# Optimization experiments

Hardware: AMD Instinct MI355X
Metric: run time of the kernel (lower is better)

Reference implementation:

```python
import jax, jax.numpy as jnp
import numpy as np

B, L, D, H, NC = 32, 1024, 256, 512, 16


def setup_inputs() -> dict:
    key = jax.random.key(0)
    ks = jax.random.split(key, 8)
    s_in = 1.0 / np.sqrt(D)
    s_h = 1.0 / np.sqrt(H)
    return {
        "x": jax.random.normal(ks[0], (B, L, D), jnp.float32),
        "W0": jax.random.normal(ks[1], (D, 4 * H), jnp.float32) * s_in,
        "b0": jnp.zeros((2 * H,), jnp.float32),
        "W1": jax.random.normal(ks[2], (H, 3 * H), jnp.float32) * s_h,
        "b1": jnp.zeros((2 * H,), jnp.float32),
        "W2": jax.random.normal(ks[3], (H, 3 * H), jnp.float32) * s_h,
        "b2": jnp.zeros((2 * H,), jnp.float32),
        "W3": jax.random.normal(ks[4], (H, 3 * H), jnp.float32) * s_h,
        "b3": jnp.zeros((2 * H,), jnp.float32),
        "Wp": jax.random.normal(ks[5], (H, H), jnp.float32) * s_h,
        "bp": jnp.zeros((H,), jnp.float32),
        "Wc": jax.random.normal(ks[6], (H, NC), jnp.float32) * s_h,
        "bc": jnp.zeros((NC,), jnp.float32),
    }


def _sru_layer(h, W, b, first):
    # h: (B, L, Din); W: (Din, kH); b: (2H,)
    k = 4 if first else 3
    Hh = W.shape[1] // k
    U = jnp.einsum('bld,dk->blk', h, W)  # (B, L, kH)
    if first:
        xt, fpre, rpre, xres = jnp.split(U, 4, axis=-1)
    else:
        xt, fpre, rpre = jnp.split(U, 3, axis=-1)
        xres = h
    bf, br = jnp.split(b, 2)
    f = jax.nn.sigmoid(fpre + bf)  # forget gate (B, L, H)
    r = jax.nn.sigmoid(rpre + br)  # reset/highway gate

    def step(c, inp):
        f_t, x_t = inp
        c = f_t * c + (1.0 - f_t) * x_t
        return c, c

    c0 = jnp.zeros((h.shape[0], Hh), h.dtype)
    _, c_seq = jax.lax.scan(step, c0, (jnp.swapaxes(f, 0, 1), jnp.swapaxes(xt, 0, 1)))
    c_seq = jnp.swapaxes(c_seq, 0, 1)  # (B, L, H)
    out = r * c_seq + (1.0 - r) * xres  # highway output
    return out, c_seq[:, -1, :]


def reference(x, W0, b0, W1, b1, W2, b2, W3, b3, Wp, bp, Wc, bc):
    h = x
    finals = []
    for W, b, first in ((W0, b0, True), (W1, b1, False), (W2, b2, False), (W3, b3, False)):
        h, cT = _sru_layer(h, W, b, first)
        finals.append(cT)
    hidden = jnp.stack(finals)  # (num_layers, B, H)
    projected = h[:, -1, :] @ Wp + bp
    output = projected @ Wc + bc
    return output, h, hidden
```

## Files before the change

kernel.cpp:

```cpp
#include <hip/hip_runtime.h>

#define DEV_INLINE __device__ __forceinline__

typedef __attribute__((ext_vector_type(8))) short bf16x8;
typedef __attribute__((ext_vector_type(4))) float f32x4;

DEV_INLINE unsigned short f2bf(float f) {
  union { float f; unsigned u; } v; v.f = f;
  unsigned r = v.u + 0x7FFFu + ((v.u >> 16) & 1u);
  return (unsigned short)(r >> 16);
}
DEV_INLINE float bf2f(unsigned short u) {
  union { unsigned u; float f; } v; v.u = ((unsigned)u) << 16;
  return v.f;
}
DEV_INLINE float sigmoidf_(float x) { return 1.0f / (1.0f + __expf(-x)); }

DEV_INLINE void gload_lds16(const void* g, void* l) {
  __builtin_amdgcn_global_load_lds(
      (const __attribute__((address_space(1))) void*)(g),
      (__attribute__((address_space(3))) void*)(l), 16, 0, 0);
}

__global__ __launch_bounds__(256)
void f32_to_bf16_kernel(const float* __restrict__ in, unsigned short* __restrict__ out, int n4) {
  int i = blockIdx.x * blockDim.x + threadIdx.x;
  if (i >= n4) return;
  const float4 v = reinterpret_cast<const float4*>(in)[i];
  ushort4 o;
  o.x = f2bf(v.x); o.y = f2bf(v.y); o.z = f2bf(v.z); o.w = f2bf(v.w);
  reinterpret_cast<ushort4*>(out)[i] = o;
}

__global__ __launch_bounds__(256)
void transpose_bf16_kernel(const float* __restrict__ W, unsigned short* __restrict__ Wt,
                           int K, int N) {
  __shared__ float tile[32][33];
  const int tx = threadIdx.x, ty = threadIdx.y;
  const int kb = blockIdx.x * 32, nb = blockIdx.y * 32;
  #pragma unroll
  for (int i = 0; i < 32; i += 8)
    tile[ty + i][tx] = W[(size_t)(kb + ty + i) * N + (nb + tx)];
  __syncthreads();
  #pragma unroll
  for (int i = 0; i < 32; i += 8)
    Wt[(size_t)(nb + ty + i) * K + (kb + tx)] = f2bf(tile[tx][ty + i]);
}

__global__ __launch_bounds__(256, 2)
void gemm_gate_kernel(const unsigned short* __restrict__ A,
                      const unsigned short* __restrict__ Bt,
                      const float* __restrict__ bias,
                      unsigned short* __restrict__ U,
                      int N, int K, int NTN) {
  __shared__ short smem[2 * 128 * 64];
  short* As = smem;
  short* Bs = smem + 128 * 64;

  const int tid = threadIdx.x;
  const int lane = tid & 63;
  const int l15 = lane & 15;
  const int l4 = lane >> 4;
  const int w = tid >> 6;
  const int wr = (w >> 1) * 64;
  const int wc = (w & 1) * 64;

  const int nwg = gridDim.x;
  const int cpx = nwg >> 3;
  const int swz = (blockIdx.x & 7) * cpx + (blockIdx.x >> 3);
  const int mtile = swz / NTN;
  const int ntile = swz - mtile * NTN;
  const int m0 = mtile * 128;
  const int n0 = ntile * 128;

  f32x4 acc[4][4];
  #pragma unroll
  for (int i = 0; i < 4; ++i)
    #pragma unroll
    for (int j = 0; j < 4; ++j)
      acc[i][j] = (f32x4){0.f, 0.f, 0.f, 0.f};

  const unsigned short* Abase = A + (size_t)m0 * K;
  const unsigned short* Bbase = Bt + (size_t)n0 * K;
  const int nsteps = K >> 6;

  for (int t = 0; t < nsteps; ++t) {
    const int k0 = t * 64;
    #pragma unroll
    for (int it = 0; it < 4; ++it) {
      int c = it * 256 + tid;
      int row = c >> 3, sl = c & 7;
      int ks = sl ^ (row & 7);
      gload_lds16(Abase + (size_t)row * K + (k0 + ks * 8), &As[c * 8]);
    }
    #pragma unroll
    for (int it = 0; it < 4; ++it) {
      int c = it * 256 + tid;
      int row = c >> 3, sl = c & 7;
      int ks = sl ^ (row & 7);
      gload_lds16(Bbase + (size_t)row * K + (k0 + ks * 8), &Bs[c * 8]);
    }
    __syncthreads();

    const bf16x8* As8 = (const bf16x8*)As;
    const bf16x8* Bs8 = (const bf16x8*)Bs;
    #pragma unroll
    for (int kk = 0; kk < 2; ++kk) {
      bf16x8 af[4], bfr[4];
      #pragma unroll
      for (int i = 0; i < 4; ++i) {
        int r = wr + i * 16 + l15;
        int phys = (kk * 4 + l4) ^ (r & 7);
        af[i] = As8[r * 8 + phys];
      }
      #pragma unroll
      for (int j = 0; j < 4; ++j) {
        int r = wc + j * 16 + l15;
        int phys = (kk * 4 + l4) ^ (r & 7);
        bfr[j] = Bs8[r * 8 + phys];
      }
      #pragma unroll
      for (int i = 0; i < 4; ++i)
        #pragma unroll
        for (int j = 0; j < 4; ++j)
          acc[i][j] = __builtin_amdgcn_mfma_f32_16x16x32_bf16(af[i], bfr[j], acc[i][j], 0, 0, 0);
    }
    __syncthreads();
  }

  short* eps = smem;
  const int EL = 144;
  #pragma unroll
  for (int p = 0; p < 2; ++p) {
    __syncthreads();
    #pragma unroll
    for (int ii = 0; ii < 2; ++ii) {
      const int i = 2 * p + ii;
      #pragma unroll
      for (int j = 0; j < 4; ++j) {
        const int cg = n0 + wc + j * 16 + l15;
        const int region = cg >> 9;
        #pragma unroll
        for (int reg = 0; reg < 4; ++reg) {
          float v = acc[i][j][reg];
          if (region == 1)      v = sigmoidf_(v + bias[cg & 511]);
          else if (region == 2) v = sigmoidf_(v + bias[512 + (cg & 511)]);
          const int lr = (wr >> 1) + ii * 16 + l4 * 4 + reg;
          const int col = (wc + j * 16 + l15) ^ (((lr >> 2) & 3) << 3);
          eps[lr * EL + col] = (short)f2bf(v);
        }
      }
    }
    __syncthreads();
    const int lr2 = tid >> 2;
    const int grow = m0 + ((lr2 >> 5) << 6) + (2 * p + ((lr2 >> 4) & 1)) * 16 + (lr2 & 15);
    const int xorv = ((lr2 >> 2) & 3) << 3;
    unsigned short* urow = U + (size_t)grow * N + n0;
    #pragma unroll
    for (int k = 0; k < 4; ++k) {
      const int col = (tid & 3) * 8 + k * 32;
      bf16x8 vv = *(const bf16x8*)&eps[lr2 * EL + (col ^ xorv)];
      *(bf16x8*)(urow + col) = vv;
    }
  }
}

__global__ __launch_bounds__(512)
void scan_kernel(const unsigned short* __restrict__ U, int N, int first,
                 const unsigned short* __restrict__ hin,
                 unsigned short* __restrict__ hout_bf,
                 float* __restrict__ hout_f32,
                 float* __restrict__ hidden) {
  const int b = blockIdx.x >> 3;
  const int hslice = blockIdx.x & 7;
  const int hv = threadIdx.x & 7;
  const int ch = threadIdx.x >> 3;
  const int h0 = (hslice << 6) + (hv << 3);
  __shared__ float sP[64 * 68];
  __shared__ float sQ[64 * 68];

  const size_t rowBase = (size_t)b * 1024 + (size_t)ch * 16;
  const unsigned short* Uxt = U + rowBase * N + h0;

  float c[8], P[8];
  #pragma unroll
  for (int j = 0; j < 8; ++j) { c[j] = 0.f; P[j] = 1.f; }
  {
    const unsigned short* px = Uxt;
    const unsigned short* pf = Uxt + 512;
    #pragma unroll 2
    for (int l = 0; l < 16; ++l) {
      bf16x8 xv = *(const bf16x8*)px;
      bf16x8 fv = *(const bf16x8*)pf;
      #pragma unroll
      for (int j = 0; j < 8; ++j) {
        float f  = bf2f((unsigned short)fv[j]);
        float xt = bf2f((unsigned short)xv[j]);
        c[j] = f * c[j] + (1.f - f) * xt;
        P[j] *= f;
      }
      px += N; pf += N;
    }
  }
  float* myP = &sP[ch * 68 + hv * 8];
  float* myQ = &sQ[ch * 68 + hv * 8];
  #pragma unroll
  for (int j = 0; j < 8; ++j) { myP[j] = P[j]; myQ[j] = c[j]; }
  __syncthreads();

  for (int s = 1; s < 64; s <<= 1) {
    float pp[8], pq[8];
    const bool act = (ch >= s);
    if (act) {
      const float* qP = &sP[(ch - s) * 68 + hv * 8];
      const float* qQ = &sQ[(ch - s) * 68 + hv * 8];
      #pragma unroll
      for (int j = 0; j < 8; ++j) { pp[j] = qP[j]; pq[j] = qQ[j]; }
    }
    __syncthreads();
    if (act) {
      #pragma unroll
      for (int j = 0; j < 8; ++j) {
        c[j] = P[j] * pq[j] + c[j];
        P[j] = P[j] * pp[j];
        myP[j] = P[j]; myQ[j] = c[j];
      }
    }
    __syncthreads();
  }

  float cc[8];
  if (ch == 0) {
    #pragma unroll
    for (int j = 0; j < 8; ++j) cc[j] = 0.f;
  } else {
    const float* qQ = &sQ[(ch - 1) * 68 + hv * 8];
    #pragma unroll
    for (int j = 0; j < 8; ++j) cc[j] = qQ[j];
  }

  const unsigned short* px = Uxt;
  const unsigned short* pf = Uxt + 512;
  const unsigned short* pr = Uxt + 1024;
  const unsigned short* pxr = first ? (Uxt + 1536) : (hin + rowBase * 512 + h0);
  const int xr_stride = first ? N : 512;
  unsigned short* ob = hout_bf ? hout_bf + rowBase * 512 + h0 : (unsigned short*)nullptr;
  float* of = hout_f32 ? hout_f32 + rowBase * 512 + h0 : (float*)nullptr;
  #pragma unroll 2
  for (int l = 0; l < 16; ++l) {
    bf16x8 xv = *(const bf16x8*)px;
    bf16x8 fv = *(const bf16x8*)pf;
    bf16x8 rv = *(const bf16x8*)pr;
    bf16x8 xrv = *(const bf16x8*)pxr;
    bf16x8 obuf;
    float o0, o1, o2, o3, o4, o5, o6, o7;
    float ofl[8];
    #pragma unroll
    for (int j = 0; j < 8; ++j) {
      float f  = bf2f((unsigned short)fv[j]);
      float xt = bf2f((unsigned short)xv[j]);
      cc[j] = f * cc[j] + (1.f - f) * xt;
      float r  = bf2f((unsigned short)rv[j]);
      float xr = bf2f((unsigned short)xrv[j]);
      float o = r * cc[j] + (1.f - r) * xr;
      obuf[j] = (short)f2bf(o);
      ofl[j] = o;
    }
    if (ob) { *(bf16x8*)ob = obuf; ob += 512; }
    if (of) {
      float4 v0 = make_float4(ofl[0], ofl[1], ofl[2], ofl[3]);
      float4 v1 = make_float4(ofl[4], ofl[5], ofl[6], ofl[7]);
      *(float4*)of = v0;
      *(float4*)(of + 4) = v1;
      of += 512;
    }
    px += N; pf += N; pr += N; pxr += xr_stride;
  }
  if (ch == 63) {
    #pragma unroll
    for (int j = 0; j < 8; ++j) hidden[(size_t)b * 512 + h0 + j] = cc[j];
  }
}

__global__ __launch_bounds__(256)
void proj_kernel(const float* __restrict__ hfull, const float* __restrict__ Wp,
                 const float* __restrict__ bp, const float* __restrict__ Wc,
                 const float* __restrict__ bc, float* __restrict__ out) {
  __shared__ float hl[512];
  __shared__ float pr[512];
  const int b = blockIdx.x, t = threadIdx.x;
  const float* hrow = hfull + ((size_t)b * 1024 + 1023) * 512;
  hl[t] = hrow[t];
  hl[t + 256] = hrow[t + 256];
  __syncthreads();
  for (int j = t; j < 512; j += 256) {
    float s = 0.f;
    for (int k = 0; k < 512; ++k) s += hl[k] * Wp[(size_t)k * 512 + j];
    pr[j] = s + bp[j];
  }
  __syncthreads();
  if (t < 16) {
    float s = 0.f;
    for (int k = 0; k < 512; ++k) s += pr[k] * Wc[k * 16 + t];
    out[b * 16 + t] = s + bc[t];
  }
}

extern "C" void kernel_launch(void* const* d_in, const int* in_sizes, int n_in,
                              void* d_out, int out_size, void* d_ws, size_t ws_size,
                              hipStream_t stream) {
  const float* x  = (const float*)d_in[0];
  const float* W0 = (const float*)d_in[1];
  const float* b0 = (const float*)d_in[2];
  const float* W1 = (const float*)d_in[3];
  const float* b1 = (const float*)d_in[4];
  const float* W2 = (const float*)d_in[5];
  const float* b2 = (const float*)d_in[6];
  const float* W3 = (const float*)d_in[7];
  const float* b3 = (const float*)d_in[8];
  const float* Wp = (const float*)d_in[9];
  const float* bp = (const float*)d_in[10];
  const float* Wc = (const float*)d_in[11];
  const float* bc = (const float*)d_in[12];

  float* out = (float*)d_out;
  float* outO = out;
  float* outH = out + 512;
  float* outHid = out + 512 + (size_t)32 * 1024 * 512;

  char* ws = (char*)d_ws;
  size_t off = 0;
  auto alloc = [&](size_t bytes) {
    void* p = ws + off;
    off += (bytes + 255) & ~(size_t)255;
    return p;
  };
  unsigned short* Wt0 = (unsigned short*)alloc((size_t)2048 * 256 * 2);
  unsigned short* Wt1 = (unsigned short*)alloc((size_t)1536 * 512 * 2);
  unsigned short* Wt2 = (unsigned short*)alloc((size_t)1536 * 512 * 2);
  unsigned short* Wt3 = (unsigned short*)alloc((size_t)1536 * 512 * 2);
  unsigned short* xbf = (unsigned short*)alloc((size_t)32768 * 256 * 2);
  unsigned short* h0  = (unsigned short*)alloc((size_t)32768 * 512 * 2);
  unsigned short* h1  = (unsigned short*)alloc((size_t)32768 * 512 * 2);
  unsigned short* Ubf = (unsigned short*)alloc((size_t)32768 * 2048 * 2);
  (void)ws_size; (void)in_sizes; (void)n_in; (void)out_size;

  f32_to_bf16_kernel<<<8192, 256, 0, stream>>>(x, xbf, 8388608 / 4);
  transpose_bf16_kernel<<<dim3(8, 64),  dim3(32, 8), 0, stream>>>(W0, Wt0, 256, 2048);
  transpose_bf16_kernel<<<dim3(16, 48), dim3(32, 8), 0, stream>>>(W1, Wt1, 512, 1536);
  transpose_bf16_kernel<<<dim3(16, 48), dim3(32, 8), 0, stream>>>(W2, Wt2, 512, 1536);
  transpose_bf16_kernel<<<dim3(16, 48), dim3(32, 8), 0, stream>>>(W3, Wt3, 512, 1536);

  gemm_gate_kernel<<<256 * 16, 256, 0, stream>>>(xbf, Wt0, b0, Ubf, 2048, 256, 16);
  scan_kernel<<<256, 512, 0, stream>>>(Ubf, 2048, 1, nullptr, h0, nullptr, outHid + 0);
  gemm_gate_kernel<<<256 * 12, 256, 0, stream>>>(h0, Wt1, b1, Ubf, 1536, 512, 12);
  scan_kernel<<<256, 512, 0, stream>>>(Ubf, 1536, 0, h0, h1, nullptr, outHid + 16384);
  gemm_gate_kernel<<<256 * 12, 256, 0, stream>>>(h1, Wt2, b2, Ubf, 1536, 512, 12);
  scan_kernel<<<256, 512, 0, stream>>>(Ubf, 1536, 0, h1, h0, nullptr, outHid + 32768);
  gemm_gate_kernel<<<256 * 12, 256, 0, stream>>>(h0, Wt3, b3, Ubf, 1536, 512, 12);
  scan_kernel<<<256, 512, 0, stream>>>(Ubf, 1536, 0, h0, nullptr, outH, outHid + 49152);

  proj_kernel<<<32, 256, 0, stream>>>(outH, Wp, bp, Wc, bc, outO);
}
```

Before: 567.6 us.

## Rewrite gate GEMM as 256x256 tile, 8-wave, double-buffered pipelined kernel

```diff
diff --git a/kernel.cpp b/kernel.cpp
--- a/kernel.cpp
+++ b/kernel.cpp
@@ -47,120 +47,125 @@
     Wt[(size_t)(nb + ty + i) * K + (kb + tx)] = f2bf(tile[tx][ty + i]);
 }
 
-__global__ __launch_bounds__(256, 2)
+
+DEV_INLINE void stage_half(int s, const unsigned short* Abase, const unsigned short* Bbase,
+                           int K, short* smem, int tid) {
+  const int u = s >> 2, j = s & 3;
+  short* dst = smem + ((u & 1) << 15) + ((j < 2) ? 16384 : 0) + ((j & 1) << 13);
+  const unsigned short* src = ((j < 2) ? Bbase : Abase) + (size_t)((j & 1) * 128) * K + u * 64;
+  #pragma unroll
+  for (int it = 0; it < 2; ++it) {
+    const int c = it * 512 + tid;
+    const int row = c >> 3;
+    const int ks = (c & 7) ^ (row & 7);
+    gload_lds16(src + (size_t)row * K + ks * 8, dst + c * 8);
+  }
+}
+
+__global__ __launch_bounds__(512, 2)
 void gemm_gate_kernel(const unsigned short* __restrict__ A,
                       const unsigned short* __restrict__ Bt,
                       const float* __restrict__ bias,
                       unsigned short* __restrict__ U,
                       int N, int K, int NTN) {
-  __shared__ short smem[2 * 128 * 64];
-  short* As = smem;
-  short* Bs = smem + 128 * 64;
-
+  __shared__ short smem[65536];
   const int tid = threadIdx.x;
   const int lane = tid & 63;
-  const int l15 = lane & 15;
-  const int l4 = lane >> 4;
+  const int l15 = lane & 15, l4 = lane >> 4;
   const int w = tid >> 6;
-  const int wr = (w >> 1) * 64;
-  const int wc = (w & 1) * 64;
+  const int wr = w >> 2, wc = w & 3;
 
   const int nwg = gridDim.x;
   const int cpx = nwg >> 3;
   const int swz = (blockIdx.x & 7) * cpx + (blockIdx.x >> 3);
   const int mtile = swz / NTN;
   const int ntile = swz - mtile * NTN;
-  const int m0 = mtile * 128;
-  const int n0 = ntile * 128;
-
-  f32x4 acc[4][4];
-  #pragma unroll
-  for (int i = 0; i < 4; ++i)
+  const int m0 = mtile * 256, n0 = ntile * 256;
+
+  const unsigned short* Abase = A + (size_t)m0 * K;
+  const unsigned short* Bbase = Bt + (size_t)n0 * K;
+  const int NT = K >> 6;
+
+  f32x4 acc[8][4];
+  #pragma unroll
+  for (int i = 0; i < 8; ++i)
     #pragma unroll
     for (int j = 0; j < 4; ++j)
       acc[i][j] = (f32x4){0.f, 0.f, 0.f, 0.f};
-
-  const unsigned short* Abase = A + (size_t)m0 * K;
-  const unsigned short* Bbase = Bt + (size_t)n0 * K;
-  const int nsteps = K >> 6;
-
-  for (int t = 0; t < nsteps; ++t) {
-    const int k0 = t * 64;
-    #pragma unroll
-    for (int it = 0; it < 4; ++it) {
-      int c = it * 256 + tid;
-      int row = c >> 3, sl = c & 7;
-      int ks = sl ^ (row & 7);
-      gload_lds16(Abase + (size_t)row * K + (k0 + ks * 8), &As[c * 8]);
-    }
-    #pragma unroll
-    for (int it = 0; it < 4; ++it) {
-      int c = it * 256 + tid;
-      int row = c >> 3, sl = c & 7;
-      int ks = sl ^ (row & 7);
-      gload_lds16(Bbase + (size_t)row * K + (k0 + ks * 8), &Bs[c * 8]);
-    }
-    __syncthreads();
-
-    const bf16x8* As8 = (const bf16x8*)As;
-    const bf16x8* Bs8 = (const bf16x8*)Bs;
-    #pragma unroll
-    for (int kk = 0; kk < 2; ++kk) {
-      bf16x8 af[4], bfr[4];
+  bf16x8 bq[4][2];
+
+  #pragma unroll
+  for (int s = 0; s < 7; ++s) stage_half(s, Abase, Bbase, K, smem, tid);
+  asm volatile("s_waitcnt vmcnt(6)" ::: "memory");
+  __builtin_amdgcn_sched_barrier(0);
+  asm volatile("s_barrier" ::: "memory");
+  __builtin_amdgcn_sched_barrier(0);
+
+#define PHASE(p_) do {                                                         \
+    const int kk_ = ((p_) - 1) & 1;                                            \
+    const int mb_ = ((p_) <= 2) ? 0 : 4;                                       \
+    const short* Ab_ = smem + ((t & 1) << 15);                                 \
+    const short* Bb_ = Ab_ + 16384;                                            \
+    bf16x8 af_[4];                                                             \
+    _Pragma("unroll")                                                          \
+    for (int i_ = 0; i_ < 4; ++i_) {                                           \
+      const int rl_ = 32 * (mb_ + i_) + 16 * wr + l15;                         \
+      af_[i_] = *(const bf16x8*)(Ab_ + rl_ * 64 + (((kk_ * 4 + l4) ^ (rl_ & 7)) << 3)); \
+    }                                                                          \
+    if ((p_) == 1) {                                                           \
+      _Pragma("unroll")                                                        \
+      for (int n_ = 0; n_ < 4; ++n_) {                                         \
+        const int rl_ = wc * 64 + 16 * n_ + l15;                               \
+        bq[n_][0] = *(const bf16x8*)(Bb_ + rl_ * 64 + (((0 + l4) ^ (rl_ & 7)) << 3)); \
+        bq[n_][1] = *(const bf16x8*)(Bb_ + rl_ * 64 + (((4 + l4) ^ (rl_ & 7)) << 3)); \
+      }                                                                        \
+    }                                                                          \
+    { const int s_ = 4 * t + 6 + (p_);                                         \
+      if (s_ < 4 * NT) stage_half(s_, Abase, Bbase, K, smem, tid); }           \
+    __builtin_amdgcn_sched_barrier(0);                                         \
+    asm volatile("s_barrier" ::: "memory");                                    \
+    __builtin_amdgcn_sched_barrier(0);                                         \
+    __builtin_amdgcn_s_setprio(1);                                             \
+    _Pragma("unroll")                                                          \
+    for (int i_ = 0; i_ < 4; ++i_)                                             \
+      _Pragma("unroll")                                                        \
+      for (int n_ = 0; n_ < 4; ++n_)                                           \
+        acc[mb_ + i_][n_] = __builtin_amdgcn_mfma_f32_16x16x32_bf16(           \
+            af_[i_], bq[n_][kk_], acc[mb_ + i_][n_], 0, 0, 0);                 \
+    __builtin_amdgcn_s_setprio(0);                                             \
+    __builtin_amdgcn_sched_barrier(0);                                         \
+    if ((p_) == 4) {                                                           \
+      if (t < NT - 2) { asm volatile("s_waitcnt vmcnt(6)" ::: "memory"); }     \
+      else            { asm volatile("s_waitcnt vmcnt(0)" ::: "memory"); }     \
+    }                                                                          \
+    asm volatile("s_barrier" ::: "memory");                                    \
+    __builtin_amdgcn_sched_barrier(0);                                         \
+  } while (0)
+
+  for (int t = 0; t < NT; ++t) {
+    PHASE(1);
+    PHASE(2);
+    PHASE(3);
+    PHASE(4);
+  }
+#undef PHASE
+
+  #pragma unroll
+  for (int m = 0; m < 8; ++m) {
+    const int grow = m0 + 32 * m + 16 * wr + l4 * 4;
+    #pragma unroll
+    for (int n = 0; n < 4; ++n) {
+      const int gcol = n0 + wc * 64 + n * 16 + l15;
+      const int region = gcol >> 9;
+      const bool gate = (region == 1) | (region == 2);
+      const float bval = (region == 1) ? bias[gcol & 511]
+                       : ((region == 2) ? bias[512 + (gcol & 511)] : 0.f);
       #pragma unroll
-      for (int i = 0; i < 4; ++i) {
-        int r = wr + i * 16 + l15;
-        int phys = (kk * 4 + l4) ^ (r & 7);
-        af[i] = As8[r * 8 + phys];
+      for (int reg = 0; reg < 4; ++reg) {
+        float v = acc[m][n][reg];
+        if (gate) v = sigmoidf_(v + bval);
+        U[(size_t)(grow + reg) * N + gcol] = f2bf(v);
       }
-      #pragma unroll
-      for (int j = 0; j < 4; ++j) {
-        int r = wc + j * 16 + l15;
-        int phys = (kk * 4 + l4) ^ (r & 7);
-        bfr[j] = Bs8[r * 8 + phys];
-      }
-      #pragma unroll
-      for (int i = 0; i < 4; ++i)
-        #pragma unroll
-        for (int j = 0; j < 4; ++j)
-          acc[i][j] = __builtin_amdgcn_mfma_f32_16x16x32_bf16(af[i], bfr[j], acc[i][j], 0, 0, 0);
-    }
-    __syncthreads();
-  }
-
-  short* eps = smem;
-  const int EL = 144;
-  #pragma unroll
-  for (int p = 0; p < 2; ++p) {
-    __syncthreads();
-    #pragma unroll
-    for (int ii = 0; ii < 2; ++ii) {
-      const int i = 2 * p + ii;
-      #pragma unroll
-      for (int j = 0; j < 4; ++j) {
-        const int cg = n0 + wc + j * 16 + l15;
-        const int region = cg >> 9;
-        #pragma unroll
-        for (int reg = 0; reg < 4; ++reg) {
-          float v = acc[i][j][reg];
-          if (region == 1)      v = sigmoidf_(v + bias[cg & 511]);
-          else if (region == 2) v = sigmoidf_(v + bias[512 + (cg & 511)]);
-          const int lr = (wr >> 1) + ii * 16 + l4 * 4 + reg;
-          const int col = (wc + j * 16 + l15) ^ (((lr >> 2) & 3) << 3);
-          eps[lr * EL + col] = (short)f2bf(v);
-        }
-      }
-    }
-    __syncthreads();
-    const int lr2 = tid >> 2;
-    const int grow = m0 + ((lr2 >> 5) << 6) + (2 * p + ((lr2 >> 4) & 1)) * 16 + (lr2 & 15);
-    const int xorv = ((lr2 >> 2) & 3) << 3;
-    unsigned short* urow = U + (size_t)grow * N + n0;
-    #pragma unroll
-    for (int k = 0; k < 4; ++k) {
-      const int col = (tid & 3) * 8 + k * 32;
-      bf16x8 vv = *(const bf16x8*)&eps[lr2 * EL + (col ^ xorv)];
-      *(bf16x8*)(urow + col) = vv;
     }
   }
 }
@@ -253,7 +258,6 @@
     bf16x8 rv = *(const bf16x8*)pr;
     bf16x8 xrv = *(const bf16x8*)pxr;
     bf16x8 obuf;
-    float o0, o1, o2, o3, o4, o5, o6, o7;
     float ofl[8];
     #pragma unroll
     for (int j = 0; j < 8; ++j) {
@@ -268,10 +272,8 @@
     }
     if (ob) { *(bf16x8*)ob = obuf; ob += 512; }
     if (of) {
-      float4 v0 = make_float4(ofl[0], ofl[1], ofl[2], ofl[3]);
-      float4 v1 = make_float4(ofl[4], ofl[5], ofl[6], ofl[7]);
-      *(float4*)of = v0;
-      *(float4*)(of + 4) = v1;
+      *(float4*)of = make_float4(ofl[0], ofl[1], ofl[2], ofl[3]);
+      *(float4*)(of + 4) = make_float4(ofl[4], ofl[5], ofl[6], ofl[7]);
       of += 512;
     }
     px += N; pf += N; pr += N; pxr += xr_stride;
@@ -351,13 +353,13 @@
   transpose_bf16_kernel<<<dim3(16, 48), dim3(32, 8), 0, stream>>>(W2, Wt2, 512, 1536);
   transpose_bf16_kernel<<<dim3(16, 48), dim3(32, 8), 0, stream>>>(W3, Wt3, 512, 1536);
 
-  gemm_gate_kernel<<<256 * 16, 256, 0, stream>>>(xbf, Wt0, b0, Ubf, 2048, 256, 16);
+  gemm_gate_kernel<<<128 * 8, 512, 0, stream>>>(xbf, Wt0, b0, Ubf, 2048, 256, 8);
   scan_kernel<<<256, 512, 0, stream>>>(Ubf, 2048, 1, nullptr, h0, nullptr, outHid + 0);
-  gemm_gate_kernel<<<256 * 12, 256, 0, stream>>>(h0, Wt1, b1, Ubf, 1536, 512, 12);
+  gemm_gate_kernel<<<128 * 6, 512, 0, stream>>>(h0, Wt1, b1, Ubf, 1536, 512, 6);
   scan_kernel<<<256, 512, 0, stream>>>(Ubf, 1536, 0, h0, h1, nullptr, outHid + 16384);
-  gemm_gate_kernel<<<256 * 12, 256, 0, stream>>>(h1, Wt2, b2, Ubf, 1536, 512, 12);
+  gemm_gate_kernel<<<128 * 6, 512, 0, stream>>>(h1, Wt2, b2, Ubf, 1536, 512, 6);
   scan_kernel<<<256, 512, 0, stream>>>(Ubf, 1536, 0, h1, h0, nullptr, outHid + 32768);
-  gemm_gate_kernel<<<256 * 12, 256, 0, stream>>>(h0, Wt3, b3, Ubf, 1536, 512, 12);
+  gemm_gate_kernel<<<128 * 6, 512, 0, stream>>>(h0, Wt3, b3, Ubf, 1536, 512, 6);
   scan_kernel<<<256, 512, 0, stream>>>(Ubf, 1536, 0, h0, nullptr, outH, outHid + 49152);
 
   proj_kernel<<<32, 256, 0, stream>>>(outH, Wp, bp, Wc, bc, outO);
```

Result: slower. 706.0 us (+24.4%).
